# Kernel optimization log

Hardware: AMD Instinct MI355X
Metric: run time of the kernel (lower is better)

The kernel has to match this reference:

```python
import jax, jax.numpy as jnp
import numpy as np

N = 64            # latent_dim
S = N + 1         # number of coupling steps: list(range(N)) + [0]
B = 131072        # batch
WIDTHS = (256, 256)


def _xavier(key, shape):
    fan_in, fan_out = shape[-2], shape[-1]
    lim = float(np.sqrt(6.0 / (fan_in + fan_out)))
    return jax.random.uniform(key, shape, jnp.float32, -lim, lim)


def setup_inputs() -> dict:
    key = jax.random.key(0)
    ks = jax.random.split(key, 6)
    x = jax.random.normal(ks[0], (B, N), jnp.float32)
    s = jax.random.normal(ks[1], (N,), jnp.float32)
    # Per-step t_block MLP params, stacked over the S steps: (N-1) -> 256 -> 256 -> 1
    W1 = _xavier(ks[2], (S, N - 1, WIDTHS[0]))
    b1 = jnp.zeros((S, WIDTHS[0]), jnp.float32)
    W2 = _xavier(ks[3], (S, WIDTHS[0], WIDTHS[1]))
    b2 = jnp.zeros((S, WIDTHS[1]), jnp.float32)
    W3 = _xavier(ks[4], (S, WIDTHS[1], 1))
    b3 = jnp.zeros((S, 1), jnp.float32)
    # Permutation index per step: Pi swaps coordinate idx with the last coordinate.
    idx = jnp.array(list(range(N)) + [0], dtype=jnp.int32)
    return dict(x=x, s=s, W1=W1, b1=b1, W2=W2, b2=b2, W3=W3, b3=b3, idx=idx)


def reference(x, s, W1, b1, W2, b2, W3, b3, idx):
    # Faithful forward_flow: each step permutes (swap column i <-> last),
    # applies additive coupling z[:, -1] += t(z[:, :-1]), and un-permutes.
    def step(z, per):
        w1, bb1, w2, bb2, w3, bb3, i = per
        # (Pi @ z.T).T == swap columns i and -1 (Pi is a symmetric row-swap of I)
        ci = z[:, i]
        z = z.at[:, i].set(z[:, -1]).at[:, -1].set(ci)
        z1 = z[:, :-1]                         # [B, N-1]
        h = jax.nn.relu(z1 @ w1 + bb1)         # [B, 256]
        h = jax.nn.relu(h @ w2 + bb2)          # [B, 256]
        t = (h @ w3 + bb3)[:, 0]               # [B]
        z = z.at[:, -1].add(t)
        # (Pi.T @ zp.T).T == same swap back (Pi.T == Pi)
        ci = z[:, i]
        z = z.at[:, i].set(z[:, -1]).at[:, -1].set(ci)
        return z, None

    z, _ = jax.lax.scan(step, x, (W1, b1, W2, b2, W3, b3, idx))
    return jnp.exp(s) * z
```

## Files before the change

kernel.cpp:

```cpp
#include <hip/hip_runtime.h>

#define B_ROWS 131072
#define NSTEP  65
#define ROWS   64
#define NBLK   (B_ROWS / ROWS)
#define THREADS 512

typedef __attribute__((ext_vector_type(8))) short short8;
typedef __attribute__((ext_vector_type(4))) float floatx4;
typedef __attribute__((ext_vector_type(4))) unsigned int uintx4;

__device__ __forceinline__ unsigned short f2bf(float f) {
    unsigned int u = __builtin_bit_cast(unsigned int, f);
    u += 0x7FFFu + ((u >> 16) & 1u);
    return (unsigned short)(u >> 16);
}

__global__ __launch_bounds__(256) void pack_w1(const float* __restrict__ W1,
                                               const float* __restrict__ b1,
                                               unsigned short* __restrict__ out) {
    int t = blockIdx.x * 256 + threadIdx.x;
    int n = t & 255, kc = (t >> 8) & 1, stp = t >> 9;
    unsigned int wbuf[16];
#pragma unroll
    for (int e = 0; e < 16; ++e) {
        int k0 = kc * 32 + e * 2, k1 = k0 + 1;
        float v0 = (k0 < 63) ? W1[((size_t)stp * 63 + k0) * 256 + n] : b1[(size_t)stp * 256 + n];
        float v1 = (k1 < 63) ? W1[((size_t)stp * 63 + k1) * 256 + n] : b1[(size_t)stp * 256 + n];
        wbuf[e] = (unsigned)f2bf(v0) | ((unsigned)f2bf(v1) << 16);
    }
    uintx4* o = (uintx4*)out;
#pragma unroll
    for (int j = 0; j < 4; ++j) {
        uintx4 u = {wbuf[j*4+0], wbuf[j*4+1], wbuf[j*4+2], wbuf[j*4+3]};
        o[(size_t)t * 4 + j] = u;
    }
}

__global__ __launch_bounds__(256) void pack_w2(const float* __restrict__ W2,
                                               unsigned short* __restrict__ out) {
    int t = blockIdx.x * 256 + threadIdx.x;
    int n = t & 255, kc = (t >> 8) & 7, stp = t >> 11;
    unsigned int wbuf[16];
#pragma unroll
    for (int e = 0; e < 16; ++e) {
        int k0 = kc * 32 + e * 2;
        float v0 = W2[((size_t)stp * 256 + k0) * 256 + n];
        float v1 = W2[((size_t)stp * 256 + k0 + 1) * 256 + n];
        wbuf[e] = (unsigned)f2bf(v0) | ((unsigned)f2bf(v1) << 16);
    }
    uintx4* o = (uintx4*)out;
#pragma unroll
    for (int j = 0; j < 4; ++j) {
        uintx4 u = {wbuf[j*4+0], wbuf[j*4+1], wbuf[j*4+2], wbuf[j*4+3]};
        o[(size_t)t * 4 + j] = u;
    }
}

__global__ __launch_bounds__(THREADS, 4) void flow_kernel(
    const float* __restrict__ x,
    const float* __restrict__ sg,
    const unsigned short* __restrict__ Wb1p,
    const unsigned short* __restrict__ Wb2p,
    const float* __restrict__ b2g,
    const float* __restrict__ w3g,
    const float* __restrict__ b3g,
    const int* __restrict__ idxg,
    float* __restrict__ out)
{
    __shared__ float  zm[ROWS][65];
    __shared__ uintx4 tileA[ROWS * 8];
    __shared__ uintx4 H1[ROWS * 32];
    __shared__ float  TR[8][ROWS];

    const int tid  = threadIdx.x;
    const int w    = tid >> 6;
    const int lane = tid & 63;
    const int q    = lane >> 4;
    const int c    = lane & 15;
    const int b0   = blockIdx.x * ROWS;

    unsigned short*     tileS = (unsigned short*)tileA;
    unsigned long long* H1u   = (unsigned long long*)H1;
    const uintx4* w1v = (const uintx4*)Wb1p;
    const uintx4* w2v = (const uintx4*)Wb2p;

#pragma unroll 4
    for (int it = 0; it < (ROWS * 64) / THREADS; ++it) {
        int flat = it * THREADS + tid;
        int row = flat >> 6, col = flat & 63;
        float v = x[(size_t)(b0 + row) * 64 + col];
        zm[row][col] = v;
        tileS[row * 64 + ((((col >> 3) ^ (row & 7)) << 3) | (col & 7))] =
            (col == 63) ? (unsigned short)0x3F80u : f2bf(v);
    }
    __syncthreads();

    if (tid < ROWS) {
        int row = tid, i0 = idxg[0];
        tileS[row * 64 + ((((i0 >> 3) ^ (row & 7)) << 3) | (i0 & 7))] = f2bf(zm[row][63]);
    }
    __syncthreads();

#pragma unroll 1
    for (int step = 0; step < NSTEP; ++step) {
        const int i = idxg[step];

        floatx4 acc[2][4];
#pragma unroll
        for (int a = 0; a < 2; ++a)
#pragma unroll
            for (int b = 0; b < 4; ++b) acc[a][b] = (floatx4){0.f, 0.f, 0.f, 0.f};

#pragma unroll
        for (int kc = 0; kc < 2; ++kc) {
            short8 bz[4], aw[2];
#pragma unroll
            for (int j = 0; j < 4; ++j)
                bz[j] = __builtin_bit_cast(short8,
                    tileA[(j * 16 + c) * 8 + ((kc * 4 + q) ^ (c & 7))]);
#pragma unroll
            for (int i4 = 0; i4 < 2; ++i4)
                aw[i4] = __builtin_bit_cast(short8,
                    w1v[((size_t)(step * 2 + kc) * 256 + w * 32 + i4 * 16 + c) * 4 + q]);
#pragma unroll
            for (int i4 = 0; i4 < 2; ++i4)
#pragma unroll
                for (int j = 0; j < 4; ++j)
                    acc[i4][j] = __builtin_amdgcn_mfma_f32_16x16x32_bf16(
                        aw[i4], bz[j], acc[i4][j], 0, 0, 0);
        }

#pragma unroll
        for (int i4 = 0; i4 < 2; ++i4) {
            int c16 = (w * 4 + i4 * 2 + (q >> 1)) ^ c;
#pragma unroll
            for (int j = 0; j < 4; ++j) {
                int row = j * 16 + c;
                float h0 = fmaxf(acc[i4][j][0], 0.f);
                float h1 = fmaxf(acc[i4][j][1], 0.f);
                float h2 = fmaxf(acc[i4][j][2], 0.f);
                float h3 = fmaxf(acc[i4][j][3], 0.f);
                unsigned d0 = (unsigned)f2bf(h0) | ((unsigned)f2bf(h1) << 16);
                unsigned d1 = (unsigned)f2bf(h2) | ((unsigned)f2bf(h3) << 16);
                H1u[(row * 32 + c16) * 2 + (q & 1)] =
                    (unsigned long long)d0 | ((unsigned long long)d1 << 32);
            }
        }
        __syncthreads();

#pragma unroll
        for (int a = 0; a < 2; ++a)
#pragma unroll
            for (int b = 0; b < 4; ++b) acc[a][b] = (floatx4){0.f, 0.f, 0.f, 0.f};

#pragma unroll
        for (int kc = 0; kc < 8; ++kc) {
            short8 bh[4], aw[2];
#pragma unroll
            for (int j = 0; j < 4; ++j)
                bh[j] = __builtin_bit_cast(short8,
                    H1[(j * 16 + c) * 32 + ((kc * 4 + q) ^ c)]);
#pragma unroll
            for (int i4 = 0; i4 < 2; ++i4)
                aw[i4] = __builtin_bit_cast(short8,
                    w2v[((size_t)(step * 8 + kc) * 256 + w * 32 + i4 * 16 + c) * 4 + q]);
#pragma unroll
            for (int i4 = 0; i4 < 2; ++i4)
#pragma unroll
                for (int j = 0; j < 4; ++j)
                    acc[i4][j] = __builtin_amdgcn_mfma_f32_16x16x32_bf16(
                        aw[i4], bh[j], acc[i4][j], 0, 0, 0);
        }

        {
            float p[4];
#pragma unroll
            for (int j = 0; j < 4; ++j) p[j] = 0.f;
#pragma unroll
            for (int i4 = 0; i4 < 2; ++i4) {
#pragma unroll
                for (int r = 0; r < 4; ++r) {
                    int col2 = step * 256 + w * 32 + i4 * 16 + q * 4 + r;
                    float bb = b2g[col2];
                    float ww = w3g[col2];
#pragma unroll
                    for (int j = 0; j < 4; ++j)
                        p[j] += fmaxf(acc[i4][j][r] + bb, 0.f) * ww;
                }
            }
#pragma unroll
            for (int j = 0; j < 4; ++j) {
                float t = p[j];
                t += __shfl_xor(t, 16, 64);
                t += __shfl_xor(t, 32, 64);
                if (q == 0) TR[w][j * 16 + c] = t;
            }
        }
        __syncthreads();

        if (tid < ROWS) {
            int row = tid;
            float t = TR[0][row] + TR[1][row] + TR[2][row] + TR[3][row]
                    + TR[4][row] + TR[5][row] + TR[6][row] + TR[7][row] + b3g[step];
            float nz = zm[row][i] + t;
            zm[row][i] = nz;
            if (i != 63)
                tileS[row * 64 + ((((i >> 3) ^ (row & 7)) << 3) | (i & 7))] = f2bf(nz);
            if (step + 1 < NSTEP) {
                int in = idxg[step + 1];
                if (in != 63)
                    tileS[row * 64 + ((((in >> 3) ^ (row & 7)) << 3) | (in & 7))] =
                        f2bf(zm[row][63]);
            }
        }
        __syncthreads();
    }

    if (tid < 64) ((float*)TR)[tid] = expf(sg[tid]);
    __syncthreads();
#pragma unroll 4
    for (int it = 0; it < (ROWS * 64) / THREADS; ++it) {
        int flat = it * THREADS + tid;
        int row = flat >> 6, col = flat & 63;
        out[(size_t)(b0 + row) * 64 + col] = ((float*)TR)[col] * zm[row][col];
    }
}

extern "C" void kernel_launch(void* const* d_in, const int* in_sizes, int n_in,
                              void* d_out, int out_size, void* d_ws, size_t ws_size,
                              hipStream_t stream) {
    const float* x  = (const float*)d_in[0];
    const float* s  = (const float*)d_in[1];
    const float* W1 = (const float*)d_in[2];
    const float* b1 = (const float*)d_in[3];
    const float* W2 = (const float*)d_in[4];
    const float* b2 = (const float*)d_in[5];
    const float* W3 = (const float*)d_in[6];
    const float* b3 = (const float*)d_in[7];
    const int* idx  = (const int*)d_in[8];
    float* out = (float*)d_out;

    char* ws = (char*)d_ws;
    const size_t W1P_BYTES = (size_t)NSTEP * 2 * 256 * 32 * 2;
    unsigned short* Wb1p = (unsigned short*)ws;
    unsigned short* Wb2p = (unsigned short*)(ws + W1P_BYTES);

    pack_w1<<<130, 256, 0, stream>>>(W1, b1, Wb1p);
    pack_w2<<<520, 256, 0, stream>>>(W2, Wb2p);
    flow_kernel<<<NBLK, THREADS, 0, stream>>>(x, s, Wb1p, Wb2p, b2, W3, b3, idx, out);
}
```

Before: 1.798 ms.

## Remove per-step barrier via redundant per-wave update and prefetch next-step W1 weights

Every wave now does the per-row coupling update for all 64 rows. Each wave writes identical values into the shared tile, which lets the trailing __syncthreads of each step be dropped. zm is written only by wave 0. Next-step W1 fragments are prefetched into registers during the current step, and the b2/w3 global loads are hoisted before the MFMA loops. bf16 packing now uses the HIP intrinsic conversion. This adds redundant work across waves and relies on benign same-value races in LDS.

```diff
diff --git a/kernel.cpp b/kernel.cpp
--- a/kernel.cpp
+++ b/kernel.cpp
@@ -1,4 +1,5 @@
 #include <hip/hip_runtime.h>
+#include <hip/hip_bf16.h>
 
 #define B_ROWS 131072
 #define NSTEP  65
@@ -14,6 +15,12 @@
     unsigned int u = __builtin_bit_cast(unsigned int, f);
     u += 0x7FFFu + ((u >> 16) & 1u);
     return (unsigned short)(u >> 16);
+}
+
+__device__ __forceinline__ unsigned pack_bf16(float lo, float hi) {
+    unsigned short l = __bfloat16_as_ushort(__float2bfloat16(lo));
+    unsigned short h = __bfloat16_as_ushort(__float2bfloat16(hi));
+    return (unsigned)l | ((unsigned)h << 16);
 }
 
 __global__ __launch_bounds__(256) void pack_w1(const float* __restrict__ W1,
@@ -102,9 +109,29 @@
     }
     __syncthreads();
 
+    short8 aw1[2][2];
+#pragma unroll
+    for (int kc = 0; kc < 2; ++kc)
+#pragma unroll
+        for (int i4 = 0; i4 < 2; ++i4)
+            aw1[kc][i4] = __builtin_bit_cast(short8,
+                w1v[((size_t)kc * 256 + w * 32 + i4 * 16 + c) * 4 + q]);
+
 #pragma unroll 1
     for (int step = 0; step < NSTEP; ++step) {
-        const int i = idxg[step];
+        const int i   = idxg[step];
+        const int inx = (step + 1 < NSTEP) ? idxg[step + 1] : 0;
+        const float b3v = b3g[step];
+
+        float bb[2][4], ww[2][4];
+#pragma unroll
+        for (int i4 = 0; i4 < 2; ++i4)
+#pragma unroll
+            for (int r = 0; r < 4; ++r) {
+                int col2 = step * 256 + w * 32 + i4 * 16 + q * 4 + r;
+                bb[i4][r] = b2g[col2];
+                ww[i4][r] = w3g[col2];
+            }
 
         floatx4 acc[2][4];
 #pragma unroll
@@ -114,21 +141,26 @@
 
 #pragma unroll
         for (int kc = 0; kc < 2; ++kc) {
-            short8 bz[4], aw[2];
+            short8 bz[4];
 #pragma unroll
             for (int j = 0; j < 4; ++j)
                 bz[j] = __builtin_bit_cast(short8,
                     tileA[(j * 16 + c) * 8 + ((kc * 4 + q) ^ (c & 7))]);
 #pragma unroll
             for (int i4 = 0; i4 < 2; ++i4)
-                aw[i4] = __builtin_bit_cast(short8,
-                    w1v[((size_t)(step * 2 + kc) * 256 + w * 32 + i4 * 16 + c) * 4 + q]);
-#pragma unroll
-            for (int i4 = 0; i4 < 2; ++i4)
 #pragma unroll
                 for (int j = 0; j < 4; ++j)
                     acc[i4][j] = __builtin_amdgcn_mfma_f32_16x16x32_bf16(
-                        aw[i4], bz[j], acc[i4][j], 0, 0, 0);
+                        aw1[kc][i4], bz[j], acc[i4][j], 0, 0, 0);
+        }
+
+        if (step + 1 < NSTEP) {
+#pragma unroll
+            for (int kc = 0; kc < 2; ++kc)
+#pragma unroll
+                for (int i4 = 0; i4 < 2; ++i4)
+                    aw1[kc][i4] = __builtin_bit_cast(short8,
+                        w1v[((size_t)((step + 1) * 2 + kc) * 256 + w * 32 + i4 * 16 + c) * 4 + q]);
         }
 
 #pragma unroll
@@ -137,12 +169,10 @@
 #pragma unroll
             for (int j = 0; j < 4; ++j) {
                 int row = j * 16 + c;
-                float h0 = fmaxf(acc[i4][j][0], 0.f);
-                float h1 = fmaxf(acc[i4][j][1], 0.f);
-                float h2 = fmaxf(acc[i4][j][2], 0.f);
-                float h3 = fmaxf(acc[i4][j][3], 0.f);
-                unsigned d0 = (unsigned)f2bf(h0) | ((unsigned)f2bf(h1) << 16);
-                unsigned d1 = (unsigned)f2bf(h2) | ((unsigned)f2bf(h3) << 16);
+                unsigned d0 = pack_bf16(fmaxf(acc[i4][j][0], 0.f),
+                                        fmaxf(acc[i4][j][1], 0.f));
+                unsigned d1 = pack_bf16(fmaxf(acc[i4][j][2], 0.f),
+                                        fmaxf(acc[i4][j][3], 0.f));
                 H1u[(row * 32 + c16) * 2 + (q & 1)] =
                     (unsigned long long)d0 | ((unsigned long long)d1 << 32);
             }
@@ -181,12 +211,9 @@
             for (int i4 = 0; i4 < 2; ++i4) {
 #pragma unroll
                 for (int r = 0; r < 4; ++r) {
-                    int col2 = step * 256 + w * 32 + i4 * 16 + q * 4 + r;
-                    float bb = b2g[col2];
-                    float ww = w3g[col2];
 #pragma unroll
                     for (int j = 0; j < 4; ++j)
-                        p[j] += fmaxf(acc[i4][j][r] + bb, 0.f) * ww;
+                        p[j] += fmaxf(acc[i4][j][r] + bb[i4][r], 0.f) * ww[i4][r];
                 }
             }
 #pragma unroll
@@ -197,26 +224,29 @@
                 if (q == 0) TR[w][j * 16 + c] = t;
             }
         }
+
+        float zold = zm[lane][i];
+        float z63  = zm[lane][63];
         __syncthreads();
 
-        if (tid < ROWS) {
-            int row = tid;
+        {
+            int row = lane;
             float t = TR[0][row] + TR[1][row] + TR[2][row] + TR[3][row]
-                    + TR[4][row] + TR[5][row] + TR[6][row] + TR[7][row] + b3g[step];
-            float nz = zm[row][i] + t;
-            zm[row][i] = nz;
+                    + TR[4][row] + TR[5][row] + TR[6][row] + TR[7][row] + b3v;
+            float nz = zold + t;
+            if (w == 0) zm[row][i] = nz;
             if (i != 63)
                 tileS[row * 64 + ((((i >> 3) ^ (row & 7)) << 3) | (i & 7))] = f2bf(nz);
             if (step + 1 < NSTEP) {
-                int in = idxg[step + 1];
-                if (in != 63)
-                    tileS[row * 64 + ((((in >> 3) ^ (row & 7)) << 3) | (in & 7))] =
-                        f2bf(zm[row][63]);
-            }
-        }
-        __syncthreads();
-    }
-
+                float z63v = (i == 63) ? nz : z63;
+                if (inx != 63)
+                    tileS[row * 64 + ((((inx >> 3) ^ (row & 7)) << 3) | (inx & 7))] =
+                        f2bf(z63v);
+            }
+        }
+    }
+
+    __syncthreads();
     if (tid < 64) ((float*)TR)[tid] = expf(sg[tid]);
     __syncthreads();
 #pragma unroll 4
```

Measured after the change: 2.522 ms. 40.3% more time.
